# Performance work log

Hardware: AMD Instinct MI355X
Metric: run time of the kernel (lower is better)

## Reference

```python
import jax, jax.numpy as jnp
import numpy as np

ROUTINGS = 3
EPS = 1e-9

def _squash(s):
    # squash along the capsule-vector (last) axis
    sq = jnp.sum(s * s, axis=-1, keepdims=True)
    return s * (sq / (1.0 + sq)) / jnp.sqrt(sq + EPS)

def setup_inputs() -> dict:
    key = jax.random.key(0)
    k1, k2 = jax.random.split(key)
    B, N, D, d = 32, 64, 128, 128  # batch, num_capsule(=input_num_capsule), dim_capsule, input_dim_capsule
    x = jax.random.normal(k1, (B, N, d), dtype=jnp.float32)
    W = jax.random.normal(k2, (1, N, N, D, d), dtype=jnp.float32)
    return {"x": x, "W": W}

def reference(x, W):
    # u[b,j,k,:] = W[0,j,k] @ x[b,j]  (faithful to broadcast matmul, N==I)
    u = jnp.einsum('jkde,bje->bjkd', W[0], x)  # (B,N,N,D)
    b = jnp.zeros_like(u)                      # routing logits carry D axis per source
    v = None
    for i in range(ROUTINGS):
        c = jax.nn.softmax(b, axis=2)
        s = jnp.sum(c * u, axis=1, keepdims=True)  # (B,1,N,D)
        v = _squash(s)
        if i < ROUTINGS - 1:
            b = b + u * v  # (inputs*outputs).sum over trailing singleton dim
    return v[:, 0, :, :, None]  # (B,N,D,1) matching torch outputs.squeeze(1)
```

## Files before the change

### kernel.cpp

```cpp
#include <hip/hip_runtime.h>

#define NB 32
#define NN 64
#define ND 128
#define NE 128
#define NK 64

typedef float  f32x4  __attribute__((ext_vector_type(4)));
typedef short  short8 __attribute__((ext_vector_type(8)));
typedef __bf16 bf16x8 __attribute__((ext_vector_type(8)));

union Frag { bf16x8 h; short8 s; };

static constexpr size_t U_BYTES = (size_t)NB * NN * ND * NK * 2;
static constexpr size_t V_BYTES = (size_t)NB * ND * NK * 4;
static constexpr size_t WS_NEED = U_BYTES + 2 * V_BYTES;

template <int CTRL, int RMASK>
__device__ __forceinline__ float dppf(float x) {
    int xi = __float_as_int(x);
    return __int_as_float(__builtin_amdgcn_update_dpp(xi, xi, CTRL, RMASK, 0xF, false));
}
__device__ __forceinline__ float wave_sum(float x) {
    x += dppf<0xB1, 0xF>(x);
    x += dppf<0x4E, 0xF>(x);
    x += dppf<0x141, 0xF>(x);
    x += dppf<0x140, 0xF>(x);
    x += dppf<0x142, 0xA>(x);
    x += dppf<0x143, 0xC>(x);
    return __int_as_float(__builtin_amdgcn_readlane(__float_as_int(x), 63));
}

__device__ __forceinline__ ushort f2bf(float f) {
    __bf16 h = (__bf16)f;
    ushort r;
    __builtin_memcpy(&r, &h, 2);
    return r;
}
__device__ __forceinline__ float bf2f(ushort r) {
    return __int_as_float(((int)r) << 16);
}
__device__ __forceinline__ void cvt8(const float4& a, const float4& b, Frag& fr) {
    fr.h[0] = (__bf16)a.x; fr.h[1] = (__bf16)a.y; fr.h[2] = (__bf16)a.z; fr.h[3] = (__bf16)a.w;
    fr.h[4] = (__bf16)b.x; fr.h[5] = (__bf16)b.y; fr.h[6] = (__bf16)b.z; fr.h[7] = (__bf16)b.w;
}

__global__ __launch_bounds__(256) void k_u(const float* __restrict__ W,
                                           const float* __restrict__ x,
                                           ushort* __restrict__ u) {
    __shared__ ushort T[4][32][72];
    const int t  = threadIdx.x;
    const int wv = t >> 6;
    const int l  = t & 63;
    const int gw = blockIdx.x * 4 + wv;
    const int j  = gw >> 7;
    const int d  = gw & 127;

    const int lr = l & 15;
    const int e0 = (l >> 4) * 8;

    const float* xb = x + (size_t)j * NE;
    const float* Wb = W + ((size_t)(j * NN) * ND + d) * NE;

    Frag a[2][4];
#pragma unroll
    for (int mt = 0; mt < 2; ++mt)
#pragma unroll
        for (int ec = 0; ec < 4; ++ec) {
            const float* p = xb + (size_t)(mt * 16 + lr) * (NN * NE) + ec * 32 + e0;
            float4 f0 = *reinterpret_cast<const float4*>(p);
            float4 f1 = *reinterpret_cast<const float4*>(p + 4);
            cvt8(f0, f1, a[mt][ec]);
        }

    f32x4 acc[2][4];
#pragma unroll
    for (int mt = 0; mt < 2; ++mt)
#pragma unroll
        for (int nt = 0; nt < 4; ++nt) acc[mt][nt] = (f32x4)0.0f;

#pragma unroll
    for (int nt = 0; nt < 4; ++nt) {
        Frag bw[4];
#pragma unroll
        for (int ec = 0; ec < 4; ++ec) {
            const float* p = Wb + (size_t)(nt * 16 + lr) * (ND * NE) + ec * 32 + e0;
            f32x4 g0 = __builtin_nontemporal_load(reinterpret_cast<const f32x4*>(p));
            f32x4 g1 = __builtin_nontemporal_load(reinterpret_cast<const f32x4*>(p + 4));
            float4 f0 = {g0[0], g0[1], g0[2], g0[3]};
            float4 f1 = {g1[0], g1[1], g1[2], g1[3]};
            cvt8(f0, f1, bw[ec]);
        }
#pragma unroll
        for (int ec = 0; ec < 4; ++ec)
#pragma unroll
            for (int mt = 0; mt < 2; ++mt)
                acc[mt][nt] = __builtin_amdgcn_mfma_f32_16x16x32_bf16(
                    a[mt][ec].s, bw[ec].s, acc[mt][nt], 0, 0, 0);
    }

    const int lq = l >> 4;
#pragma unroll
    for (int mt = 0; mt < 2; ++mt)
#pragma unroll
        for (int nt = 0; nt < 4; ++nt)
#pragma unroll
            for (int r = 0; r < 4; ++r)
                T[wv][mt * 16 + lq * 4 + r][nt * 16 + lr] = f2bf(acc[mt][nt][r]);
    __syncthreads();

    const int b2 = l >> 1;
    const int kh = (l & 1) * 32;
    ushort* up = u + (((size_t)b2 * NN + j) * ND + d) * NK + kh;
    const ushort* tp = &T[wv][b2][kh];
#pragma unroll
    for (int i = 0; i < 4; ++i) {
        short8 v = *reinterpret_cast<const short8*>(tp + i * 8);
        *reinterpret_cast<short8*>(up + i * 8) = v;
    }
}

__global__ __launch_bounds__(512) void k_route(const ushort* __restrict__ u,
                                               const float* __restrict__ Vsum,
                                               float* __restrict__ s,
                                               int first) {
    __shared__ float P[8][8][65];
    const int b  = blockIdx.x >> 4;
    const int dg = blockIdx.x & 15;
    const int t  = threadIdx.x;
    const int wv = t >> 6;
    const int l  = t & 63;

    float sacc[8];
#pragma unroll
    for (int dd = 0; dd < 8; ++dd) sacc[dd] = 0.0f;

    const ushort* ub = u + (((size_t)b * NN + wv * 8) * ND + dg * 8) * NK + l;

    if (first) {
        for (int jj = 0; jj < 8; ++jj) {
            const ushort* up = ub + (size_t)jj * (ND * NK);
#pragma unroll
            for (int dd = 0; dd < 8; ++dd) sacc[dd] += bf2f(up[dd * NK]);
        }
#pragma unroll
        for (int dd = 0; dd < 8; ++dd) sacc[dd] *= (1.0f / 64.0f);
    } else {
        float vs[8];
#pragma unroll
        for (int dd = 0; dd < 8; ++dd)
            vs[dd] = Vsum[((size_t)b * ND + dg * 8 + dd) * NK + l];

        for (int jj = 0; jj < 8; ++jj) {
            const ushort* up = ub + (size_t)jj * (ND * NK);
            float uv[8];
#pragma unroll
            for (int dd = 0; dd < 8; ++dd) uv[dd] = bf2f(up[dd * NK]);
#pragma unroll
            for (int dd = 0; dd < 8; ++dd) {
                float p = __expf(uv[dd] * vs[dd] - 32.0f);
                float q = wave_sum(p);
                sacc[dd] = fmaf(p * __builtin_amdgcn_rcpf(q), uv[dd], sacc[dd]);
            }
        }
    }

#pragma unroll
    for (int dd = 0; dd < 8; ++dd) P[wv][dd][l] = sacc[dd];
    __syncthreads();

    const int dd = t >> 6;
    const int k  = t & 63;
    float r = P[0][dd][k];
#pragma unroll
    for (int w2 = 1; w2 < 8; ++w2) r += P[w2][dd][k];
    s[((size_t)b * ND + dg * 8 + dd) * NK + k] = r;
}

__global__ __launch_bounds__(256) void k_squash(const float* __restrict__ s,
                                                float* __restrict__ Vsum,
                                                float* __restrict__ out,
                                                int mode) {
    const int t  = threadIdx.x;
    const int gw = blockIdx.x * 4 + (t >> 6);
    const int b  = gw >> 6;
    const int k  = gw & 63;
    const int l  = t & 63;

    const float s0 = s[((size_t)b * ND + l) * NK + k];
    const float s1 = s[((size_t)b * ND + l + 64) * NK + k];
    float sq    = wave_sum(fmaf(s0, s0, s1 * s1));
    float scale = (sq / (1.0f + sq)) * rsqrtf(sq + 1e-9f);
    float v0 = s0 * scale, v1 = s1 * scale;
    if (mode == 2) {
        float* op = out + ((size_t)b * NN + k) * ND;
        op[l]      = v0;
        op[l + 64] = v1;
    } else if (mode == 0) {
        float* vp = Vsum + (size_t)b * ND * NK + k;
        vp[(size_t)l * NK]        = v0;
        vp[(size_t)(l + 64) * NK] = v1;
    } else {
        float* vp = Vsum + (size_t)b * ND * NK + k;
        vp[(size_t)l * NK]        += v0;
        vp[(size_t)(l + 64) * NK] += v1;
    }
}

extern "C" void kernel_launch(void* const* d_in, const int* in_sizes, int n_in,
                              void* d_out, int out_size, void* d_ws, size_t ws_size,
                              hipStream_t stream) {
    (void)in_sizes; (void)n_in; (void)out_size;
    const float* x = (const float*)d_in[0];
    const float* W = (const float*)d_in[1];
    float* out = (float*)d_out;

    if (ws_size < WS_NEED) return;
    char* ws = (char*)d_ws;
    ushort* u   = (ushort*)ws;
    float* Vsum = (float*)(ws + U_BYTES);
    float* s    = (float*)(ws + U_BYTES + V_BYTES);

    k_u<<<dim3(2048), dim3(256), 0, stream>>>(W, x, u);
    for (int it = 0; it < 3; ++it) {
        k_route<<<dim3(512), dim3(512), 0, stream>>>(u, Vsum, s, it == 0 ? 1 : 0);
        k_squash<<<dim3(512), dim3(256), 0, stream>>>(s, Vsum, out, it);
    }
}
```

Measured before the change: 149.0 us.

## Stream W through LDS with double-buffered async global_load_lds in k_u

Replaces the direct per-lane nontemporal W loads in the u-projection kernel with async global-to-LDS copies into a per-wave double buffer. It waits on vmcnt explicitly so the next chunk's fetch overlaps the bf16 conversion and MFMA work on the current chunk, and adds an occupancy hint of 3 blocks per CU. The aim is to hide the latency of reading W, which is the dominant memory stream. It costs 32KB of extra LDS per block plus hand-placed waitcnt and sched barriers, and it drops the nontemporal hint.

```diff
diff --git a/kernel.cpp b/kernel.cpp
--- a/kernel.cpp
+++ b/kernel.cpp
@@ -15,6 +15,11 @@
 static constexpr size_t U_BYTES = (size_t)NB * NN * ND * NK * 2;
 static constexpr size_t V_BYTES = (size_t)NB * ND * NK * 4;
 static constexpr size_t WS_NEED = U_BYTES + 2 * V_BYTES;
+
+#define GLOAD16(g, l)                                                   \
+    __builtin_amdgcn_global_load_lds(                                   \
+        (const __attribute__((address_space(1))) void*)(g),             \
+        (__attribute__((address_space(3))) void*)(l), 16, 0, 0)
 
 template <int CTRL, int RMASK>
 __device__ __forceinline__ float dppf(float x) {
@@ -45,9 +50,10 @@
     fr.h[4] = (__bf16)b.x; fr.h[5] = (__bf16)b.y; fr.h[6] = (__bf16)b.z; fr.h[7] = (__bf16)b.w;
 }
 
-__global__ __launch_bounds__(256) void k_u(const float* __restrict__ W,
-                                           const float* __restrict__ x,
-                                           ushort* __restrict__ u) {
+__global__ __launch_bounds__(256, 3) void k_u(const float* __restrict__ W,
+                                              const float* __restrict__ x,
+                                              ushort* __restrict__ u) {
+    __shared__ float  Wl[4][2][1024];
     __shared__ ushort T[4][32][72];
     const int t  = threadIdx.x;
     const int wv = t >> 6;
@@ -57,21 +63,38 @@
     const int d  = gw & 127;
 
     const int lr = l & 15;
-    const int e0 = (l >> 4) * 8;
+    const int lh = l >> 4;
+    const int e0 = lh * 8;
 
     const float* xb = x + (size_t)j * NE;
-    const float* Wb = W + ((size_t)(j * NN) * ND + d) * NE;
-
-    Frag a[2][4];
+    float4 xf[2][4][2];
 #pragma unroll
     for (int mt = 0; mt < 2; ++mt)
 #pragma unroll
         for (int ec = 0; ec < 4; ++ec) {
             const float* p = xb + (size_t)(mt * 16 + lr) * (NN * NE) + ec * 32 + e0;
-            float4 f0 = *reinterpret_cast<const float4*>(p);
-            float4 f1 = *reinterpret_cast<const float4*>(p + 4);
-            cvt8(f0, f1, a[mt][ec]);
-        }
+            xf[mt][ec][0] = *reinterpret_cast<const float4*>(p);
+            xf[mt][ec][1] = *reinterpret_cast<const float4*>(p + 4);
+        }
+    asm volatile("s_waitcnt vmcnt(0)" ::: "memory");
+    __builtin_amdgcn_sched_barrier(0);
+    Frag a[2][4];
+#pragma unroll
+    for (int mt = 0; mt < 2; ++mt)
+#pragma unroll
+        for (int ec = 0; ec < 4; ++ec) cvt8(xf[mt][ec][0], xf[mt][ec][1], a[mt][ec]);
+
+    const char* Wg = (const char*)W + ((size_t)(j * NN) * ND + d) * (NE * 4);
+#define STAGE(c, buf)                                                       \
+    {                                                                       \
+        const int nt_ = (c) >> 1, eh_ = (c) & 1;                            \
+        const char* gp_ = Wg + (size_t)(nt_ * 16 + lr) * 65536 + eh_ * 256; \
+        _Pragma("unroll") for (int i_ = 0; i_ < 4; ++i_)                    \
+            GLOAD16(gp_ + (i_ * 4 + lh) * 16, &Wl[wv][buf][i_ * 256]);      \
+    }
+
+    STAGE(0, 0);
+    STAGE(1, 1);
 
     f32x4 acc[2][4];
 #pragma unroll
@@ -80,33 +103,45 @@
         for (int nt = 0; nt < 4; ++nt) acc[mt][nt] = (f32x4)0.0f;
 
 #pragma unroll
-    for (int nt = 0; nt < 4; ++nt) {
-        Frag bw[4];
-#pragma unroll
-        for (int ec = 0; ec < 4; ++ec) {
-            const float* p = Wb + (size_t)(nt * 16 + lr) * (ND * NE) + ec * 32 + e0;
-            f32x4 g0 = __builtin_nontemporal_load(reinterpret_cast<const f32x4*>(p));
-            f32x4 g1 = __builtin_nontemporal_load(reinterpret_cast<const f32x4*>(p + 4));
-            float4 f0 = {g0[0], g0[1], g0[2], g0[3]};
-            float4 f1 = {g1[0], g1[1], g1[2], g1[3]};
-            cvt8(f0, f1, bw[ec]);
-        }
-#pragma unroll
-        for (int ec = 0; ec < 4; ++ec)
+    for (int c = 0; c < 8; ++c) {
+        const int nt = c >> 1, eh = c & 1, buf = c & 1;
+        if (c < 7) { asm volatile("s_waitcnt vmcnt(4)" ::: "memory"); }
+        else       { asm volatile("s_waitcnt vmcnt(0)" ::: "memory"); }
+        __builtin_amdgcn_sched_barrier(0);
+
+        const float* cb = &Wl[wv][buf][0];
+        f32x4 g[2][2];
+#pragma unroll
+        for (int ec = 0; ec < 2; ++ec) {
+            const int sl = (ec * 8 + lh * 2) * 64 + lr * 4;
+            g[ec][0] = *reinterpret_cast<const f32x4*>(cb + sl);
+            g[ec][1] = *reinterpret_cast<const f32x4*>(cb + sl + 64);
+        }
+        asm volatile("s_waitcnt lgkmcnt(0)" ::: "memory");
+        __builtin_amdgcn_sched_barrier(0);
+        if (c < 6) STAGE(c + 2, buf);
+
+#pragma unroll
+        for (int ec = 0; ec < 2; ++ec) {
+            Frag bw;
+            float4 f0 = {g[ec][0][0], g[ec][0][1], g[ec][0][2], g[ec][0][3]};
+            float4 f1 = {g[ec][1][0], g[ec][1][1], g[ec][1][2], g[ec][1][3]};
+            cvt8(f0, f1, bw);
 #pragma unroll
             for (int mt = 0; mt < 2; ++mt)
                 acc[mt][nt] = __builtin_amdgcn_mfma_f32_16x16x32_bf16(
-                    a[mt][ec].s, bw[ec].s, acc[mt][nt], 0, 0, 0);
-    }
-
-    const int lq = l >> 4;
+                    a[mt][eh * 2 + ec].s, bw.s, acc[mt][nt], 0, 0, 0);
+        }
+    }
+#undef STAGE
+
 #pragma unroll
     for (int mt = 0; mt < 2; ++mt)
 #pragma unroll
         for (int nt = 0; nt < 4; ++nt)
 #pragma unroll
             for (int r = 0; r < 4; ++r)
-                T[wv][mt * 16 + lq * 4 + r][nt * 16 + lr] = f2bf(acc[mt][nt][r]);
+                T[wv][mt * 16 + lh * 4 + r][nt * 16 + lr] = f2bf(acc[mt][nt][r]);
     __syncthreads();
 
     const int b2 = l >> 1;
```

Result: faster. 123.3 us (-17.3%).

## Software-pipeline W loads in k_u with triple buffering and relayout u

Applied to the files above, without the earlier changes.

Rewrites the k_u projection loop into eight explicit stages that triple-buffer W register fragments, issuing the next loads before the current MFMAs. Sched barriers pin that order, and launch bounds now request 3 blocks per SM. The loads drop nontemporal hints. The u buffer layout moves from [b][j][d][k] to [j][d][b][k], so each wave in k_u writes one contiguous block, and k_route indexing is updated to match. The extra live registers may limit occupancy, and k_route now reads u with larger strides.

```diff
diff --git a/kernel.cpp b/kernel.cpp
--- a/kernel.cpp
+++ b/kernel.cpp
@@ -12,7 +12,7 @@
 
 union Frag { bf16x8 h; short8 s; };
 
-static constexpr size_t U_BYTES = (size_t)NB * NN * ND * NK * 2;
+static constexpr size_t U_BYTES = (size_t)NN * ND * NB * NK * 2;
 static constexpr size_t V_BYTES = (size_t)NB * ND * NK * 4;
 static constexpr size_t WS_NEED = U_BYTES + 2 * V_BYTES;
 
@@ -40,14 +40,14 @@
 __device__ __forceinline__ float bf2f(ushort r) {
     return __int_as_float(((int)r) << 16);
 }
-__device__ __forceinline__ void cvt8(const float4& a, const float4& b, Frag& fr) {
-    fr.h[0] = (__bf16)a.x; fr.h[1] = (__bf16)a.y; fr.h[2] = (__bf16)a.z; fr.h[3] = (__bf16)a.w;
-    fr.h[4] = (__bf16)b.x; fr.h[5] = (__bf16)b.y; fr.h[6] = (__bf16)b.z; fr.h[7] = (__bf16)b.w;
-}
-
-__global__ __launch_bounds__(256) void k_u(const float* __restrict__ W,
-                                           const float* __restrict__ x,
-                                           ushort* __restrict__ u) {
+__device__ __forceinline__ void cvt8f(const f32x4& a, const f32x4& b, Frag& fr) {
+    fr.h[0] = (__bf16)a[0]; fr.h[1] = (__bf16)a[1]; fr.h[2] = (__bf16)a[2]; fr.h[3] = (__bf16)a[3];
+    fr.h[4] = (__bf16)b[0]; fr.h[5] = (__bf16)b[1]; fr.h[6] = (__bf16)b[2]; fr.h[7] = (__bf16)b[3];
+}
+
+__global__ __launch_bounds__(256, 3) void k_u(const float* __restrict__ W,
+                                              const float* __restrict__ x,
+                                              ushort* __restrict__ u) {
     __shared__ ushort T[4][32][72];
     const int t  = threadIdx.x;
     const int wv = t >> 6;
@@ -57,61 +57,92 @@
     const int d  = gw & 127;
 
     const int lr = l & 15;
-    const int e0 = (l >> 4) * 8;
+    const int lh = l >> 4;
 
     const float* xb = x + (size_t)j * NE;
-    const float* Wb = W + ((size_t)(j * NN) * ND + d) * NE;
-
     Frag a[2][4];
+    {
+        f32x4 xf[2][4][2];
+#pragma unroll
+        for (int mt = 0; mt < 2; ++mt)
+#pragma unroll
+            for (int ec = 0; ec < 4; ++ec) {
+                const float* p = xb + (size_t)(mt * 16 + lr) * (NN * NE) + ec * 32 + lh * 8;
+                xf[mt][ec][0] = *reinterpret_cast<const f32x4*>(p);
+                xf[mt][ec][1] = *reinterpret_cast<const f32x4*>(p + 4);
+            }
+#pragma unroll
+        for (int mt = 0; mt < 2; ++mt)
+#pragma unroll
+            for (int ec = 0; ec < 4; ++ec) cvt8f(xf[mt][ec][0], xf[mt][ec][1], a[mt][ec]);
+    }
+
+    const float* pB = W + (((size_t)j * NN + lr) * ND + d) * NE + lh * 8;
+
+#define LOADSC(sc, B)                                                          \
+    {                                                                          \
+        const float* p_ = pB + (size_t)((sc) >> 1) * (16 * ND * NE) +          \
+                          ((sc) & 1) * 64;                                     \
+        B[0] = *reinterpret_cast<const f32x4*>(p_);                            \
+        B[1] = *reinterpret_cast<const f32x4*>(p_ + 4);                        \
+        B[2] = *reinterpret_cast<const f32x4*>(p_ + 32);                       \
+        B[3] = *reinterpret_cast<const f32x4*>(p_ + 36);                       \
+    }
+
+    f32x4 B0[4], B1[4], B2[4];
+    LOADSC(0, B0);
+    LOADSC(1, B1);
+    LOADSC(2, B2);
+    __builtin_amdgcn_sched_barrier(0);
+
+    f32x4 acc[2][4];
 #pragma unroll
     for (int mt = 0; mt < 2; ++mt)
 #pragma unroll
-        for (int ec = 0; ec < 4; ++ec) {
-            const float* p = xb + (size_t)(mt * 16 + lr) * (NN * NE) + ec * 32 + e0;
-            float4 f0 = *reinterpret_cast<const float4*>(p);
-            float4 f1 = *reinterpret_cast<const float4*>(p + 4);
-            cvt8(f0, f1, a[mt][ec]);
-        }
-
-    f32x4 acc[2][4];
+        for (int nt = 0; nt < 4; ++nt) acc[mt][nt] = (f32x4)0.0f;
+
+#define STEP(sc, Bc, PRE)                                                      \
+    {                                                                          \
+        Frag bw0, bw1;                                                         \
+        cvt8f(Bc[0], Bc[1], bw0);                                              \
+        cvt8f(Bc[2], Bc[3], bw1);                                              \
+        if (PRE) LOADSC((sc) + 3, Bc);                                         \
+        __builtin_amdgcn_sched_barrier(0);                                     \
+        const int nt_ = (sc) >> 1;                                             \
+        const int e0_ = ((sc) & 1) * 2;                                        \
+        acc[0][nt_] = __builtin_amdgcn_mfma_f32_16x16x32_bf16(                 \
+            a[0][e0_].s, bw0.s, acc[0][nt_], 0, 0, 0);                         \
+        acc[1][nt_] = __builtin_amdgcn_mfma_f32_16x16x32_bf16(                 \
+            a[1][e0_].s, bw0.s, acc[1][nt_], 0, 0, 0);                         \
+        acc[0][nt_] = __builtin_amdgcn_mfma_f32_16x16x32_bf16(                 \
+            a[0][e0_ + 1].s, bw1.s, acc[0][nt_], 0, 0, 0);                     \
+        acc[1][nt_] = __builtin_amdgcn_mfma_f32_16x16x32_bf16(                 \
+            a[1][e0_ + 1].s, bw1.s, acc[1][nt_], 0, 0, 0);                     \
+    }
+
+    STEP(0, B0, 1)
+    STEP(1, B1, 1)
+    STEP(2, B2, 1)
+    STEP(3, B0, 1)
+    STEP(4, B1, 1)
+    STEP(5, B2, 0)
+    STEP(6, B0, 0)
+    STEP(7, B1, 0)
+#undef STEP
+#undef LOADSC
+
 #pragma unroll
     for (int mt = 0; mt < 2; ++mt)
 #pragma unroll
-        for (int nt = 0; nt < 4; ++nt) acc[mt][nt] = (f32x4)0.0f;
-
-#pragma unroll
-    for (int nt = 0; nt < 4; ++nt) {
-        Frag bw[4];
-#pragma unroll
-        for (int ec = 0; ec < 4; ++ec) {
-            const float* p = Wb + (size_t)(nt * 16 + lr) * (ND * NE) + ec * 32 + e0;
-            f32x4 g0 = __builtin_nontemporal_load(reinterpret_cast<const f32x4*>(p));
-            f32x4 g1 = __builtin_nontemporal_load(reinterpret_cast<const f32x4*>(p + 4));
-            float4 f0 = {g0[0], g0[1], g0[2], g0[3]};
-            float4 f1 = {g1[0], g1[1], g1[2], g1[3]};
-            cvt8(f0, f1, bw[ec]);
-        }
-#pragma unroll
-        for (int ec = 0; ec < 4; ++ec)
-#pragma unroll
-            for (int mt = 0; mt < 2; ++mt)
-                acc[mt][nt] = __builtin_amdgcn_mfma_f32_16x16x32_bf16(
-                    a[mt][ec].s, bw[ec].s, acc[mt][nt], 0, 0, 0);
-    }
-
-    const int lq = l >> 4;
-#pragma unroll
-    for (int mt = 0; mt < 2; ++mt)
-#pragma unroll
         for (int nt = 0; nt < 4; ++nt)
 #pragma unroll
             for (int r = 0; r < 4; ++r)
-                T[wv][mt * 16 + lq * 4 + r][nt * 16 + lr] = f2bf(acc[mt][nt][r]);
+                T[wv][mt * 16 + lh * 4 + r][nt * 16 + lr] = f2bf(acc[mt][nt][r]);
     __syncthreads();
 
     const int b2 = l >> 1;
     const int kh = (l & 1) * 32;
-    ushort* up = u + (((size_t)b2 * NN + j) * ND + d) * NK + kh;
+    ushort* up = u + (((size_t)j * ND + d) * NB + b2) * NK + kh;
     const ushort* tp = &T[wv][b2][kh];
 #pragma unroll
     for (int i = 0; i < 4; ++i) {
@@ -135,13 +166,15 @@
 #pragma unroll
     for (int dd = 0; dd < 8; ++dd) sacc[dd] = 0.0f;
 
-    const ushort* ub = u + (((size_t)b * NN + wv * 8) * ND + dg * 8) * NK + l;
+    const size_t JS = (size_t)ND * NB * NK;
+    const ushort* ub = u + ((size_t)(wv * 8) * ND + dg * 8) * (NB * NK) +
+                       (size_t)b * NK + l;
 
     if (first) {
         for (int jj = 0; jj < 8; ++jj) {
-            const ushort* up = ub + (size_t)jj * (ND * NK);
-#pragma unroll
-            for (int dd = 0; dd < 8; ++dd) sacc[dd] += bf2f(up[dd * NK]);
+            const ushort* up = ub + jj * JS;
+#pragma unroll
+            for (int dd = 0; dd < 8; ++dd) sacc[dd] += bf2f(up[dd * (NB * NK)]);
         }
 #pragma unroll
         for (int dd = 0; dd < 8; ++dd) sacc[dd] *= (1.0f / 64.0f);
@@ -152,10 +185,10 @@
             vs[dd] = Vsum[((size_t)b * ND + dg * 8 + dd) * NK + l];
 
         for (int jj = 0; jj < 8; ++jj) {
-            const ushort* up = ub + (size_t)jj * (ND * NK);
+            const ushort* up = ub + jj * JS;
             float uv[8];
 #pragma unroll
-            for (int dd = 0; dd < 8; ++dd) uv[dd] = bf2f(up[dd * NK]);
+            for (int dd = 0; dd < 8; ++dd) uv[dd] = bf2f(up[dd * (NB * NK)]);
 #pragma unroll
             for (int dd = 0; dd < 8; ++dd) {
                 float p = __expf(uv[dd] * vs[dd] - 32.0f);
```

Result: faster. 122.7 us (-17.6%).
